# Optimization experiments

Hardware: AMD Instinct MI355X
Metric: run time of the kernel (lower is better)

The kernel has to match this reference:

```python
import jax, jax.numpy as jnp
import numpy as np

# Winograd F(2x2, 3x3) transform matrices, copied verbatim from the source
# (note: G[1,2] is 1.2 in the original code, not 0.5 -- replicated faithfully).
B_MAT = jnp.array([[1, 0, -1, 0], [0, 1, 1, 0], [0, -1, 1, 0], [0, 1, 0, -1]], dtype=jnp.float32)
G_MAT = jnp.array([[1.0, 0.0, 0.0], [0.5, 0.5, 1.2], [0.5, -0.5, 0.5], [0.0, 0.0, 1.0]], dtype=jnp.float32)
AT_MAT = jnp.array([[1, 1, 1, 0], [0, 1, -1, -1]], dtype=jnp.float32)


def setup_inputs() -> dict:
    key = jax.random.key(0)
    k1, k2 = jax.random.split(key)
    x = jax.random.normal(k1, (64, 64, 64, 64), dtype=jnp.float32)        # [B, C, H, W]
    filters = jax.random.normal(k2, (64, 64, 3, 3), dtype=jnp.float32)    # [F, C, 3, 3]
    return {"x": x, "filters": filters}


def winograd_forward(x, filters):
    bs, C, H, W = x.shape
    F = filters.shape[0]
    m, r = 2, 3
    alpha = m + r - 1          # 4
    over = r - 1               # 2 (tile stride)
    T = (W - alpha) // over + 1
    p = bs * T * T

    # U[f,c] = G @ g @ G^T   -> [F, C, 4, 4]
    U = jnp.einsum('ij,fcjk,lk->fcil', G_MAT, filters, G_MAT)

    # Extract all 4x4 input tiles with stride 2: [C, B, T, T, 4, 4]
    xt = jnp.transpose(x, (1, 0, 2, 3))                         # [C, B, H, W]
    win = (jnp.arange(T) * over)[:, None] + jnp.arange(alpha)[None, :]  # [T, 4]
    patches = xt[:, :, win[:, None, :, None], win[None, :, None, :]]    # [C,B,T,T,4,4]

    # V[c,b] = B^T @ d @ B, flattened with b = batch*T*T + row*T + col
    V = jnp.einsum('ji,cbtujk,kl->cbtuil', B_MAT, patches, B_MAT)
    V = V.reshape(C, p, alpha, alpha)

    # Faithful to the source bug: M[f, j] is only accumulated for j < T
    # (the loop is `for j in range(tiles)` instead of range(p)); rest stay zero.
    Mpart = jnp.einsum('fcab,cjab->fjab', U, V[:, :T])          # [F, T, 4, 4]
    M = jnp.zeros((F, p, alpha, alpha), x.dtype).at[:, :T].set(Mpart)

    # Faithful to the source: Y tile index b = f*T*T + k*T + l (depends on the
    # filter index, not the batch index), so every batch gets the same tiles.
    idx = (jnp.arange(F) * T * T)[:, None] + jnp.arange(T * T)[None, :]  # [F, T*T]
    Msel = M[jnp.arange(F)[:, None], idx]                        # [F, T*T, 4, 4]

    # Inverse transform: A^T @ M @ A -> [F, T*T, 2, 2]
    Yt = jnp.einsum('ij,ftjk,kl->ftil', AT_MAT, Msel, AT_MAT.T)
    out_h = H - r + 1
    Yt = Yt.reshape(F, T, T, m, m).transpose(0, 1, 3, 2, 4).reshape(F, T * m, T * m)
    # Original allocates Y as [F, B, H-2, H-2]; with H == W they match T*m.
    Y = jnp.broadcast_to(Yt[:, None, :, :], (F, bs, out_h, out_h))
    return jnp.transpose(Y, (1, 0, 2, 3))                        # [B, F, H-2, H-2]


def reference(x, filters):
    return winograd_forward(x, filters)
```

## Files before the change

### kernel.cpp

```cpp
#include <hip/hip_runtime.h>


__global__ void winograd_small_kernel(const float* __restrict__ x,
                                      const float* __restrict__ filters,
                                      float* __restrict__ ws) {
    const int u = blockIdx.x;
    const int c = threadIdx.x;

    const float G[4][3]  = {{1.0f, 0.0f, 0.0f},
                            {0.5f, 0.5f, 1.2f},
                            {0.5f,-0.5f, 0.5f},
                            {0.0f, 0.0f, 1.0f}};
    const float Bm[4][4] = {{1.f, 0.f,-1.f, 0.f},
                            {0.f, 1.f, 1.f, 0.f},
                            {0.f,-1.f, 1.f, 0.f},
                            {0.f, 1.f, 0.f,-1.f}};

    float g[3][3];
#pragma unroll
    for (int j = 0; j < 3; ++j)
#pragma unroll
        for (int k = 0; k < 3; ++k)
            g[j][k] = filters[c * 9 + j * 3 + k];

    float t1[4][3];
#pragma unroll
    for (int i = 0; i < 4; ++i)
#pragma unroll
        for (int k = 0; k < 3; ++k) {
            float s = 0.f;
#pragma unroll
            for (int j = 0; j < 3; ++j) s += G[i][j] * g[j][k];
            t1[i][k] = s;
        }
    float U[4][4];
#pragma unroll
    for (int i = 0; i < 4; ++i)
#pragma unroll
        for (int l = 0; l < 4; ++l) {
            float s = 0.f;
#pragma unroll
            for (int k = 0; k < 3; ++k) s += t1[i][k] * G[l][k];
            U[i][l] = s;
        }

    float d[4][4];
#pragma unroll
    for (int j = 0; j < 4; ++j)
#pragma unroll
        for (int k = 0; k < 4; ++k)
            d[j][k] = x[c * 4096 + j * 64 + 2 * u + k];

    float t2[4][4];
#pragma unroll
    for (int i = 0; i < 4; ++i)
#pragma unroll
        for (int k = 0; k < 4; ++k) {
            float s = 0.f;
#pragma unroll
            for (int j = 0; j < 4; ++j) s += Bm[j][i] * d[j][k];
            t2[i][k] = s;
        }
    float V[4][4];
#pragma unroll
    for (int i = 0; i < 4; ++i)
#pragma unroll
        for (int l = 0; l < 4; ++l) {
            float s = 0.f;
#pragma unroll
            for (int k = 0; k < 4; ++k) s += t2[i][k] * Bm[k][l];
            V[i][l] = s;
        }

    __shared__ float red[16][64];
#pragma unroll
    for (int i = 0; i < 4; ++i)
#pragma unroll
        for (int l = 0; l < 4; ++l)
            red[i * 4 + l][c] = U[i][l] * V[i][l];
    __syncthreads();

    __shared__ float M[16];
    if (c < 16) {
        float s = 0.f;
        for (int t = 0; t < 64; ++t) s += red[c][t];
        M[c] = s;
    }
    __syncthreads();

    if (c == 0) {
        const float AT[2][4] = {{1.f, 1.f, 1.f, 0.f},
                                {0.f, 1.f,-1.f,-1.f}};
        float t3[2][4];
#pragma unroll
        for (int i = 0; i < 2; ++i)
#pragma unroll
            for (int k = 0; k < 4; ++k) {
                float s = 0.f;
#pragma unroll
                for (int j = 0; j < 4; ++j) s += AT[i][j] * M[j * 4 + k];
                t3[i][k] = s;
            }
#pragma unroll
        for (int i = 0; i < 2; ++i)
#pragma unroll
            for (int l = 0; l < 2; ++l) {
                float s = 0.f;
#pragma unroll
                for (int k = 0; k < 4; ++k) s += t3[i][k] * AT[l][k];
                ws[i * 62 + 2 * u + l] = s;
            }
    }
}

__global__ void fill_out_kernel(const float4* __restrict__ ws4,
                                float4* __restrict__ out4) {
    const int i4 = blockIdx.x * blockDim.x + threadIdx.x;
    const int rem = i4 % 61504;
    float4 v = make_float4(0.f, 0.f, 0.f, 0.f);
    if (rem < 31) v = ws4[rem];
    out4[i4] = v;
}

extern "C" void kernel_launch(void* const* d_in, const int* in_sizes, int n_in,
                              void* d_out, int out_size, void* d_ws, size_t ws_size,
                              hipStream_t stream) {
    const float* x       = (const float*)d_in[0];
    const float* filters = (const float*)d_in[1];
    float* out = (float*)d_out;
    float* ws  = (float*)d_ws;

    winograd_small_kernel<<<31, 64, 0, stream>>>(x, filters, ws);

    const int total4 = 3936256;
    fill_out_kernel<<<total4 / 256, 256, 0, stream>>>((const float4*)ws,
                                                      (float4*)out);
}
```

Measured before the change: 105.2 us.

## Fuse Winograd compute into output fill kernel with redundant per-block compute

Merges the small Winograd kernel and the zero-fill/broadcast kernel into one launch. Only the blocks whose range covers the start of a batch slice recompute the 31 nonzero tiles locally in shared memory (64 such blocks, each doing the full channel reduction). All other blocks simply write zeros. This removes one kernel launch and the workspace round trip, at the cost of 64-fold redundant compute in a few blocks that may become stragglers.

After: 130.9 us. +24.5%, slower.

```diff
diff --git a/kernel.cpp b/kernel.cpp
--- a/kernel.cpp
+++ b/kernel.cpp
@@ -1,125 +1,106 @@
 #include <hip/hip_runtime.h>
 
 
-__global__ void winograd_small_kernel(const float* __restrict__ x,
-                                      const float* __restrict__ filters,
-                                      float* __restrict__ ws) {
-    const int u = blockIdx.x;
-    const int c = threadIdx.x;
+static __device__ const float dG[4][3] = {{1.0f, 0.0f, 0.0f},
+                                          {0.5f, 0.5f, 1.2f},
+                                          {0.5f,-0.5f, 0.5f},
+                                          {0.0f, 0.0f, 1.0f}};
+static __device__ const float dB[4][4] = {{1.f, 0.f,-1.f, 0.f},
+                                          {0.f, 1.f, 1.f, 0.f},
+                                          {0.f,-1.f, 1.f, 0.f},
+                                          {0.f, 1.f, 0.f,-1.f}};
 
-    const float G[4][3]  = {{1.0f, 0.0f, 0.0f},
-                            {0.5f, 0.5f, 1.2f},
-                            {0.5f,-0.5f, 0.5f},
-                            {0.0f, 0.0f, 1.0f}};
-    const float Bm[4][4] = {{1.f, 0.f,-1.f, 0.f},
-                            {0.f, 1.f, 1.f, 0.f},
-                            {0.f,-1.f, 1.f, 0.f},
-                            {0.f, 1.f, 0.f,-1.f}};
+__global__ __launch_bounds__(256) void winograd_fused(
+        const float* __restrict__ x,
+        const float* __restrict__ filters,
+        float4* __restrict__ out4) {
+    const int baseI = blockIdx.x << 8;
+    const int t = threadIdx.x;
 
-    float g[3][3];
-#pragma unroll
-    for (int j = 0; j < 3; ++j)
-#pragma unroll
-        for (int k = 0; k < 3; ++k)
-            g[j][k] = filters[c * 9 + j * 3 + k];
+    const int b = (baseI + 61503) / 61504;
+    const bool special = (b < 64) && (b * 61504 < baseI + 256);
 
-    float t1[4][3];
-#pragma unroll
-    for (int i = 0; i < 4; ++i)
-#pragma unroll
-        for (int k = 0; k < 3; ++k) {
+    __shared__ float sU[64][16];
+    __shared__ float sM[31][16];
+    __shared__ float sY[124];
+
+    if (special) {
+        for (int idx = t; idx < 1024; idx += 256) {
+            const int c = idx >> 4, e = idx & 15;
+            const int i = e >> 2, l = e & 3;
+            const float* g = filters + c * 9;
             float s = 0.f;
 #pragma unroll
-            for (int j = 0; j < 3; ++j) s += G[i][j] * g[j][k];
-            t1[i][k] = s;
+            for (int j = 0; j < 3; ++j)
+#pragma unroll
+                for (int k = 0; k < 3; ++k)
+                    s += dG[i][j] * dG[l][k] * g[j * 3 + k];
+            sU[c][e] = s;
         }
-    float U[4][4];
+        __syncthreads();
+
+        for (int task = t; task < 496; task += 256) {
+            const int u = task >> 4, e = task & 15;
+            const int i = e >> 2, l = e & 3;
+            float wv[4][4];
 #pragma unroll
-    for (int i = 0; i < 4; ++i)
+            for (int j = 0; j < 4; ++j)
 #pragma unroll
-        for (int l = 0; l < 4; ++l) {
-            float s = 0.f;
+                for (int k = 0; k < 4; ++k)
+                    wv[j][k] = dB[j][i] * dB[k][l];
+            float acc = 0.f;
+            for (int c = 0; c < 64; ++c) {
+                const float* xp = x + c * 4096 + 2 * u;
+                float v = 0.f;
 #pragma unroll
-            for (int k = 0; k < 3; ++k) s += t1[i][k] * G[l][k];
-            U[i][l] = s;
+                for (int j = 0; j < 4; ++j)
+#pragma unroll
+                    for (int k = 0; k < 4; ++k)
+                        v += wv[j][k] * xp[j * 64 + k];
+                acc += sU[c][e] * v;
+            }
+            sM[u][e] = acc;
         }
+        __syncthreads();
 
-    float d[4][4];
+        if (t < 31) {
+            const int u = t;
+            const float AT[2][4] = {{1.f, 1.f, 1.f, 0.f},
+                                    {0.f, 1.f,-1.f,-1.f}};
+            float t3[2][4];
 #pragma unroll
-    for (int j = 0; j < 4; ++j)
+            for (int i = 0; i < 2; ++i)
 #pragma unroll
-        for (int k = 0; k < 4; ++k)
-            d[j][k] = x[c * 4096 + j * 64 + 2 * u + k];
+                for (int k = 0; k < 4; ++k) {
+                    float s = 0.f;
+#pragma unroll
+                    for (int j = 0; j < 4; ++j) s += AT[i][j] * sM[u][j * 4 + k];
+                    t3[i][k] = s;
+                }
+#pragma unroll
+            for (int i = 0; i < 2; ++i)
+#pragma unroll
+                for (int l = 0; l < 2; ++l) {
+                    float s = 0.f;
+#pragma unroll
+                    for (int k = 0; k < 4; ++k) s += t3[i][k] * AT[l][k];
+                    sY[i * 62 + 2 * u + l] = s;
+                }
+        }
+        __syncthreads();
+    }
 
-    float t2[4][4];
-#pragma unroll
-    for (int i = 0; i < 4; ++i)
-#pragma unroll
-        for (int k = 0; k < 4; ++k) {
-            float s = 0.f;
-#pragma unroll
-            for (int j = 0; j < 4; ++j) s += Bm[j][i] * d[j][k];
-            t2[i][k] = s;
+    float4 v = make_float4(0.f, 0.f, 0.f, 0.f);
+    if (special) {
+        const int rem = (baseI + t) - b * 61504;
+        if (rem >= 0 && rem < 31) {
+            v.x = sY[4 * rem + 0];
+            v.y = sY[4 * rem + 1];
+            v.z = sY[4 * rem + 2];
+            v.w = sY[4 * rem + 3];
         }
-    float V[4][4];
-#pragma unroll
-    for (int i = 0; i < 4; ++i)
-#pragma unroll
-        for (int l = 0; l < 4; ++l) {
-            float s = 0.f;
-#pragma unroll
-            for (int k = 0; k < 4; ++k) s += t2[i][k] * Bm[k][l];
-            V[i][l] = s;
-        }
-
-    __shared__ float red[16][64];
-#pragma unroll
-    for (int i = 0; i < 4; ++i)
-#pragma unroll
-        for (int l = 0; l < 4; ++l)
-            red[i * 4 + l][c] = U[i][l] * V[i][l];
-    __syncthreads();
-
-    __shared__ float M[16];
-    if (c < 16) {
-        float s = 0.f;
-        for (int t = 0; t < 64; ++t) s += red[c][t];
-        M[c] = s;
     }
-    __syncthreads();
-
-    if (c == 0) {
-        const float AT[2][4] = {{1.f, 1.f, 1.f, 0.f},
-                                {0.f, 1.f,-1.f,-1.f}};
-        float t3[2][4];
-#pragma unroll
-        for (int i = 0; i < 2; ++i)
-#pragma unroll
-            for (int k = 0; k < 4; ++k) {
-                float s = 0.f;
-#pragma unroll
-                for (int j = 0; j < 4; ++j) s += AT[i][j] * M[j * 4 + k];
-                t3[i][k] = s;
-            }
-#pragma unroll
-        for (int i = 0; i < 2; ++i)
-#pragma unroll
-            for (int l = 0; l < 2; ++l) {
-                float s = 0.f;
-#pragma unroll
-                for (int k = 0; k < 4; ++k) s += t3[i][k] * AT[l][k];
-                ws[i * 62 + 2 * u + l] = s;
-            }
-    }
-}
-
-__global__ void fill_out_kernel(const float4* __restrict__ ws4,
-                                float4* __restrict__ out4) {
-    const int i4 = blockIdx.x * blockDim.x + threadIdx.x;
-    const int rem = i4 % 61504;
-    float4 v = make_float4(0.f, 0.f, 0.f, 0.f);
-    if (rem < 31) v = ws4[rem];
-    out4[i4] = v;
+    out4[baseI + t] = v;
 }
 
 extern "C" void kernel_launch(void* const* d_in, const int* in_sizes, int n_in,
@@ -127,12 +108,7 @@
                               hipStream_t stream) {
     const float* x       = (const float*)d_in[0];
     const float* filters = (const float*)d_in[1];
-    float* out = (float*)d_out;
-    float* ws  = (float*)d_ws;
+    float4* out = (float4*)d_out;
 
-    winograd_small_kernel<<<31, 64, 0, stream>>>(x, filters, ws);
-
-    const int total4 = 3936256;
-    fill_out_kernel<<<total4 / 256, 256, 0, stream>>>((const float4*)ws,
-                                                      (float4*)out);
+    winograd_fused<<<15376, 256, 0, stream>>>(x, filters, out);
 }
```
